# Kernel optimization log

Measured on AMD Instinct MI355X. Metric: run time of the kernel, lower is better.

Reference implementation:

```python
import jax, jax.numpy as jnp
import numpy as np
import math

B, T, D = 8, 1024, 1024
N, L = 256, 768
H = 16
TE = 2048  # time_embed_dim
EPS = 1e-5


def _ln(x, g, b):
    mu = jnp.mean(x, axis=-1, keepdims=True)
    var = jnp.mean(jnp.square(x - mu), axis=-1, keepdims=True)
    return (x - mu) * jax.lax.rsqrt(var + EPS) * g + b


def setup_inputs() -> dict:
    key = jax.random.key(0)
    ks = jax.random.split(key, 16)
    s = lambda fan_in: 1.0 / math.sqrt(fan_in)
    return {
        "x": jax.random.normal(ks[0], (B, T, D), jnp.float32),
        "xf": jax.random.normal(ks[1], (B, N, L), jnp.float32),
        "emb": jax.random.normal(ks[2], (B, TE), jnp.float32),
        "ln_g": jnp.ones((D,), jnp.float32),
        "ln_b": jnp.zeros((D,), jnp.float32),
        "cln_g": jnp.ones((L,), jnp.float32),
        "cln_b": jnp.zeros((L,), jnp.float32),
        "Wq": jax.random.normal(ks[3], (D, D), jnp.float32) * s(D),
        "bq": jnp.zeros((D,), jnp.float32),
        "Wk": jax.random.normal(ks[4], (L, D), jnp.float32) * s(L),
        "bk": jnp.zeros((D,), jnp.float32),
        "Wv": jax.random.normal(ks[5], (L, D), jnp.float32) * s(L),
        "bv": jnp.zeros((D,), jnp.float32),
        "sln_g": jnp.ones((D,), jnp.float32),
        "sln_b": jnp.zeros((D,), jnp.float32),
        "Wemb": jax.random.normal(ks[6], (TE, 2 * D), jnp.float32) * s(TE),
        "bemb": jnp.zeros((2 * D,), jnp.float32),
        "Wout": jax.random.normal(ks[7], (D, D), jnp.float32) * s(D) * 0.02,
        "bout": jnp.zeros((D,), jnp.float32),
    }


def reference(x, xf, emb, ln_g, ln_b, cln_g, cln_b, Wq, bq, Wk, bk, Wv, bv,
              sln_g, sln_b, Wemb, bemb, Wout, bout):
    # x: (B,T,D), xf: (B,N,L), emb: (B,TE)
    hd = D // H
    q = (_ln(x, ln_g, ln_b) @ Wq + bq).reshape(B, T, H, hd)
    xf_n = _ln(xf, cln_g, cln_b)
    k = (xf_n @ Wk + bk).reshape(B, N, H, hd)
    v = (xf_n @ Wv + bv).reshape(B, N, H, hd)
    # scores: (B,T,N,H); note: scaled by sqrt(D//H)
    att = jnp.einsum('bthd,bnhd->btnh', q, k) / math.sqrt(hd)
    w = jax.nn.softmax(att, axis=2)  # softmax over conditioning tokens N
    y = jnp.einsum('btnh,bnhd->bthd', w, v).reshape(B, T, D)
    # StylizationBlock (dropout = 0)
    emb_out = jax.nn.silu(emb) @ Wemb + bemb  # (B, 2D)
    scale, shift = jnp.split(emb_out[:, None, :], 2, axis=2)
    h = _ln(y, sln_g, sln_b) * (1.0 + scale) + shift
    h = jax.nn.silu(h) @ Wout + bout
    return x + h
```

## Files before the change

### kernel.cpp

```cpp
#include <hip/hip_runtime.h>
#include <hip/hip_bf16.h>

typedef __hip_bfloat16 bf16;
typedef unsigned short ushort;
typedef unsigned char uchar;
typedef long i64;
typedef __attribute__((ext_vector_type(4))) float f32x4;

#define B_ 8
#define T_ 1024
#define D_ 1024
#define N_ 256
#define L_ 768
#define H_ 16
#define HD_ 64
#define TE_ 2048

__device__ __forceinline__ void gld16(const void* g, void* l) {
    __builtin_amdgcn_global_load_lds((const __attribute__((address_space(1))) void*)g,
                                     (__attribute__((address_space(3))) void*)l,
                                     16, 0, 0);
}

__device__ __forceinline__ float bitf(unsigned u) { return __uint_as_float(u); }

__device__ __forceinline__ int pk4_fp8(float a, float b, float c, float d) {
    int p = __builtin_amdgcn_cvt_pk_fp8_f32(a, b, 0, false);
    p = __builtin_amdgcn_cvt_pk_fp8_f32(c, d, p, true);
    return p;
}
__device__ __forceinline__ uchar pk1_fp8(float a) {
    int p = __builtin_amdgcn_cvt_pk_fp8_f32(a, a, 0, false);
    return (uchar)(p & 0xff);
}
__device__ __forceinline__ float dec8(uchar b) {
    int e = (b >> 3) & 15, m = b & 7;
    float mag = e ? (float)(8 + m) * bitf((unsigned)(117 + e) << 23)
                  : (float)m * bitf(118u << 23);
    return (b & 0x80) ? -mag : mag;
}

__global__ __launch_bounds__(256) void prep_kernel(
        const float* __restrict__ x, const float* __restrict__ xf,
        const float* __restrict__ g1, const float* __restrict__ b1,
        const float* __restrict__ g2, const float* __restrict__ b2,
        const float* __restrict__ Wq, const float* __restrict__ Wk,
        const float* __restrict__ Wv, const float* __restrict__ Wo,
        const float* __restrict__ emb, const float* __restrict__ Wemb,
        uchar* __restrict__ xn8, uchar* __restrict__ xfn8,
        uchar* __restrict__ wq8, uchar* __restrict__ wk8,
        uchar* __restrict__ wv8, uchar* __restrict__ wo8,
        float* __restrict__ part) {
    __shared__ __align__(16) char smem[16384];
    int bid = blockIdx.x;
    int tid = threadIdx.x;
    if (bid < 10240) {
        const float *rp, *g, *bb; uchar* op; int cols;
        if (bid < B_ * T_) {
            rp = x + (size_t)bid * D_; g = g1; bb = b1; op = xn8 + (size_t)bid * D_; cols = D_;
        } else {
            int r = bid - B_ * T_;
            rp = xf + (size_t)r * L_; g = g2; bb = b2; op = xfn8 + (size_t)r * L_; cols = L_;
        }
        float* ps  = (float*)smem;
        float* ps2 = ps + 4;
        float* st  = ps + 8;
        bool act = tid * 4 < cols;
        float4 v = act ? *(const float4*)&rp[tid * 4] : make_float4(0.f, 0.f, 0.f, 0.f);
        float s = v.x + v.y + v.z + v.w;
        float s2 = v.x * v.x + v.y * v.y + v.z * v.z + v.w * v.w;
        for (int off = 32; off; off >>= 1) {
            s  += __shfl_down(s,  off, 64);
            s2 += __shfl_down(s2, off, 64);
        }
        int wid = tid >> 6, lid = tid & 63;
        if (lid == 0) { ps[wid] = s; ps2[wid] = s2; }
        __syncthreads();
        if (tid == 0) {
            float t = ps[0] + ps[1] + ps[2] + ps[3];
            float t2 = ps2[0] + ps2[1] + ps2[2] + ps2[3];
            float m = t / cols;
            float var = t2 / cols - m * m;
            st[0] = m; st[1] = rsqrtf(var + 1e-5f);
        }
        __syncthreads();
        if (!act) return;
        float mu = st[0], rstd = st[1];
        float4 gv = *(const float4*)&g[tid * 4];
        float4 bv = *(const float4*)&bb[tid * 4];
        float o0 = (v.x - mu) * rstd * gv.x + bv.x;
        float o1 = (v.y - mu) * rstd * gv.y + bv.y;
        float o2 = (v.z - mu) * rstd * gv.z + bv.z;
        float o3 = (v.w - mu) * rstd * gv.w + bv.w;
        *(int*)&op[tid * 4] = pk4_fp8(o0, o1, o2, o3);
    } else if (bid < 11136) {
        uchar (*t)[65] = (uchar(*)[65])smem;
        int id = bid - 10240;
        int xb = id & 15, y = id >> 4;
        const float* W; uchar* Wt; int K, ky;
        if (y < 16)      { W = Wq; Wt = wq8; K = 1024; ky = y; }
        else if (y < 28) { W = Wk; Wt = wk8; K = 768;  ky = y - 16; }
        else if (y < 40) { W = Wv; Wt = wv8; K = 768;  ky = y - 28; }
        else             { W = Wo; Wt = wo8; K = 1024; ky = y - 40; }
        int k0 = ky * 64, n0 = xb * 64;
#pragma unroll
        for (int i = 0; i < 16; i++) {
            int e = tid + i * 256;
            int r = e >> 6, c = e & 63;
            t[r][c] = pk1_fp8(W[(size_t)(k0 + r) * D_ + n0 + c]);
        }
        __syncthreads();
#pragma unroll
        for (int i = 0; i < 4; i++) {
            int e = tid + i * 256;
            int r = e >> 4, cg = (e & 15) * 4;
            unsigned u = (unsigned)t[cg][r] | ((unsigned)t[cg + 1][r] << 8)
                       | ((unsigned)t[cg + 2][r] << 16) | ((unsigned)t[cg + 3][r] << 24);
            *(unsigned*)&Wt[(size_t)(n0 + r) * K + k0 + cg] = u;
        }
    } else {
        float* se  = (float*)smem;
        float* red = (float*)(smem + 8192);
        int id = bid - 11136;
        int j0 = (id & 31) * 64;
        int ks = id >> 5;
        int tx = tid & 15, ty = tid >> 4;
        int w = tid >> 6, lane = tid & 63;
#pragma unroll
        for (int b = 0; b < 8; b++) {
            float xv = emb[b * TE_ + ks * 256 + tid];
            se[b * 256 + tid] = xv / (1.f + __expf(-xv));
        }
        __syncthreads();
        float acc[8][4] = {};
#pragma unroll 4
        for (int i = 0; i < 16; i++) {
            int e = ty + 16 * i;
            float4 wv = *(const float4*)&Wemb[(size_t)(ks * 256 + e) * 2048 + j0 + tx * 4];
#pragma unroll
            for (int b = 0; b < 8; b++) {
                float s = se[b * 256 + e];
                acc[b][0] += s * wv.x; acc[b][1] += s * wv.y;
                acc[b][2] += s * wv.z; acc[b][3] += s * wv.w;
            }
        }
#pragma unroll
        for (int b = 0; b < 8; b++)
#pragma unroll
            for (int m = 0; m < 4; m++) {
                float v = acc[b][m];
                v += __shfl_down(v, 32, 64);
                v += __shfl_down(v, 16, 64);
                if (lane < 16) red[(w * 8 + b) * 64 + lane * 4 + m] = v;
            }
        __syncthreads();
        for (int o = tid; o < 512; o += 256) {
            int b = o >> 6, jl = o & 63;
            float s = red[(0 * 8 + b) * 64 + jl] + red[(1 * 8 + b) * 64 + jl]
                    + red[(2 * 8 + b) * 64 + jl] + red[(3 * 8 + b) * 64 + jl];
            part[((size_t)ks * 8 + b) * 2048 + j0 + jl] = s;
        }
    }
}

template <int MODE>
__device__ __forceinline__ void gemm_body(const uchar* __restrict__ Ap,
                                          const uchar* __restrict__ Bp,
                                          const float* __restrict__ bias,
                                          const float* __restrict__ res,
                                          void* __restrict__ Cout,
                                          int m0, int n0, int Ncols, int K,
                                          uchar* Ash, uchar* Bsh) {
    int tid = threadIdx.x;
    int w = tid >> 6, lane = tid & 63;
    int quad = lane >> 4, l15 = lane & 15;
    int wm = (w >> 1) * 64, wn = (w & 1) * 64;
    int lr8 = lane >> 3;
    int sc  = lane & 7;
    int gc  = sc ^ lr8;
    f32x4 acc[4][4] = {};
    for (int kt = 0; kt < K; kt += 128) {
#pragma unroll
        for (int j = 0; j < 4; j++) {
            int rbase = w * 32 + j * 8;
            gld16(&Ap[(size_t)(m0 + rbase + lr8) * K + kt + gc * 16], &Ash[rbase * 128]);
        }
#pragma unroll
        for (int j = 0; j < 4; j++) {
            int rbase = w * 32 + j * 8;
            gld16(&Bp[(size_t)(n0 + rbase + lr8) * K + kt + gc * 16], &Bsh[rbase * 128]);
        }
        __syncthreads();
#pragma unroll
        for (int kh = 0; kh < 4; kh++) {
            int c4 = kh * 2 + (quad >> 1);
            int sub = (quad & 1) * 8;
            int pos = (c4 ^ (l15 & 7)) * 16 + sub;
            i64 af[4], bfr[4];
#pragma unroll
            for (int mt = 0; mt < 4; mt++)
                af[mt] = *(const i64*)&Ash[(wm + mt * 16 + l15) * 128 + pos];
#pragma unroll
            for (int nt = 0; nt < 4; nt++)
                bfr[nt] = *(const i64*)&Bsh[(wn + nt * 16 + l15) * 128 + pos];
#pragma unroll
            for (int mt = 0; mt < 4; mt++)
#pragma unroll
                for (int nt = 0; nt < 4; nt++)
                    acc[mt][nt] = __builtin_amdgcn_mfma_f32_16x16x32_fp8_fp8(af[mt], bfr[nt], acc[mt][nt], 0, 0, 0);
        }
        __syncthreads();
    }
#pragma unroll
    for (int mt = 0; mt < 4; mt++) {
#pragma unroll
        for (int nt = 0; nt < 4; nt++) {
#pragma unroll
            for (int reg = 0; reg < 4; reg++) {
                int row = m0 + wm + mt * 16 + quad * 4 + reg;
                int col = n0 + wn + nt * 16 + l15;
                float v = acc[mt][nt][reg] + bias[col];
                if (MODE == 1) {
                    v += res[(size_t)row * Ncols + col];
                    ((float*)Cout)[(size_t)row * Ncols + col] = v;
                } else if (MODE == 0) {
                    ((uchar*)Cout)[(size_t)row * Ncols + col] = pk1_fp8(v);
                } else {
                    int b = row >> 8, n = row & 255;
                    int h = col >> 6, d = col & 63;
                    size_t addr = ((size_t)(b * 16 + h)) * 16384 + (size_t)d * 256
                                + (((n >> 4) ^ (d & 15)) * 16) + (n & 15);
                    ((uchar*)Cout)[addr] = pk1_fp8(v);
                }
            }
        }
    }
}

__global__ __launch_bounds__(256) void qkv_gemm(const uchar* __restrict__ xn8,
                                                const uchar* __restrict__ xfn8,
                                                const uchar* __restrict__ wq8,
                                                const uchar* __restrict__ wk8,
                                                const uchar* __restrict__ wv8,
                                                const float* __restrict__ bq,
                                                const float* __restrict__ bk,
                                                const float* __restrict__ bv,
                                                uchar* __restrict__ q8,
                                                uchar* __restrict__ k8,
                                                uchar* __restrict__ vT8,
                                                const float* __restrict__ part,
                                                const float* __restrict__ bemb,
                                                float* __restrict__ embo) {
    __shared__ __align__(16) uchar Ash[128 * 128];
    __shared__ __align__(16) uchar Bsh[128 * 128];
    int bid = blockIdx.x;
    if (bid < 512) {
        gemm_body<0>(xn8, wq8, bq, nullptr, q8,
                     (bid & 63) * 128, (bid >> 6) * 128, D_, D_, Ash, Bsh);
    } else if (bid < 640) {
        int id = bid - 512;
        gemm_body<0>(xfn8, wk8, bk, nullptr, k8,
                     (id & 15) * 128, (id >> 4) * 128, D_, L_, Ash, Bsh);
    } else if (bid < 768) {
        int id = bid - 640;
        gemm_body<2>(xfn8, wv8, bv, nullptr, vT8,
                     (id & 15) * 128, (id >> 4) * 128, D_, L_, Ash, Bsh);
    } else {
        int o = (bid - 768) * 256 + threadIdx.x;
        int b = o >> 11, j = o & 2047;
        float s = bemb[j];
#pragma unroll
        for (int ks = 0; ks < 8; ks++) s += part[((size_t)ks * 8 + b) * 2048 + j];
        embo[o] = s;
    }
}

__global__ __launch_bounds__(256) void out_gemm(const uchar* __restrict__ a8,
                                                const uchar* __restrict__ wo8,
                                                const float* __restrict__ bout,
                                                const float* __restrict__ x,
                                                float* __restrict__ out) {
    __shared__ __align__(16) uchar Ash[128 * 128];
    __shared__ __align__(16) uchar Bsh[128 * 128];
    int bid = blockIdx.x;
    gemm_body<1>(a8, wo8, bout, x, out,
                 (bid & 63) * 128, (bid >> 6) * 128, D_, D_, Ash, Bsh);
}

__global__ __launch_bounds__(256) void attn_mfma(const uchar* __restrict__ q8,
                                                 const uchar* __restrict__ k8,
                                                 const uchar* __restrict__ vT8,
                                                 uchar* __restrict__ y8) {
    __shared__ __align__(16) uchar KV[16384];
    __shared__ __align__(16) uchar P[16384];
    int tid = threadIdx.x;
    int w = tid >> 6, lane = tid & 63;
    int quad = lane >> 4, l15 = lane & 15;
    int t0 = blockIdx.x * 64;
    int bh = blockIdx.y;
    int b = bh >> 4, h = bh & 15;
    int lln = lane >> 3, sp = lane & 7;

#pragma unroll
    for (int j = 0; j < 4; j++) {
        int dn = w * 32 + j * 8 + lln;
        int c8 = sp ^ (dn & 7);
        int n = dn * 2 + (c8 >> 2);
        gld16(&k8[(size_t)(b * N_ + n) * D_ + h * 64 + (c8 & 3) * 16],
              &KV[(w * 32 + j * 8) * 128]);
    }
#pragma unroll
    for (int j = 0; j < 2; j++) {
        int r = w * 16 + j * 8 + lln;
        int c = (sp ^ (r & 7)) & 3;
        gld16(&q8[(size_t)(b * T_ + t0 + r) * D_ + h * 64 + c * 16],
              &P[(w * 16 + j * 8) * 128]);
    }
    __syncthreads();

    int qrow = w * 16 + l15;
    i64 aq[2];
#pragma unroll
    for (int kk2 = 0; kk2 < 2; kk2++) {
        int chunk = kk2 * 2 + (quad >> 1);
        aq[kk2] = *(const i64*)&P[qrow * 128 + ((chunk ^ (qrow & 7)) * 16) + (quad & 1) * 8];
    }
    f32x4 sf[16];
#pragma unroll
    for (int nt = 0; nt < 16; nt++) {
        int n = nt * 16 + l15;
        int dn = n >> 1, hn = n & 1;
        int c80 = (hn * 4 + 0 + (quad >> 1)) ^ (dn & 7);
        int c81 = (hn * 4 + 2 + (quad >> 1)) ^ (dn & 7);
        i64 b0 = *(const i64*)&KV[dn * 128 + c80 * 16 + (quad & 1) * 8];
        i64 b1 = *(const i64*)&KV[dn * 128 + c81 * 16 + (quad & 1) * 8];
        f32x4 z = {};
        f32x4 t = __builtin_amdgcn_mfma_f32_16x16x32_fp8_fp8(aq[0], b0, z, 0, 0, 0);
        sf[nt] = __builtin_amdgcn_mfma_f32_16x16x32_fp8_fp8(aq[1], b1, t, 0, 0, 0);
    }
    __syncthreads();

    const uchar* vbase = vT8 + (size_t)(b * 16 + h) * 16384;
#pragma unroll
    for (int j = 0; j < 4; j++) {
        gld16(&vbase[(w * 4 + j) * 1024 + lane * 16], &KV[(w * 4 + j) * 1024]);
    }

    const float scale = 0.125f;
    float sm[4] = {0.f, 0.f, 0.f, 0.f};
#pragma unroll
    for (int nt = 0; nt < 16; nt++)
#pragma unroll
        for (int reg = 0; reg < 4; reg++) {
            float e = __expf(sf[nt][reg] * scale);
            sf[nt][reg] = e;
            sm[reg] += e;
        }
#pragma unroll
    for (int off = 1; off < 16; off <<= 1)
#pragma unroll
        for (int reg = 0; reg < 4; reg++)
            sm[reg] += __shfl_xor(sm[reg], off, 64);
    float inv[4];
#pragma unroll
    for (int reg = 0; reg < 4; reg++) inv[reg] = 1.f / sm[reg];

#pragma unroll
    for (int nt = 0; nt < 16; nt++)
#pragma unroll
        for (int reg = 0; reg < 4; reg++) {
            int r = w * 16 + quad * 4 + reg;
            int n = nt * 16 + l15;
            P[r * 256 + (((n >> 4) ^ (r & 15)) * 16) + (n & 15)] = pk1_fp8(sf[nt][reg]);
        }
    __syncthreads();

    f32x4 of[4] = {};
    int prow = w * 16 + l15;
#pragma unroll
    for (int kk = 0; kk < 8; kk++) {
        int ck = kk * 2 + (quad >> 1);
        i64 ap = *(const i64*)&P[prow * 256 + ((ck ^ (prow & 15)) * 16) + (quad & 1) * 8];
#pragma unroll
        for (int dt = 0; dt < 4; dt++) {
            int d = dt * 16 + l15;
            i64 bv = *(const i64*)&KV[d * 256 + ((ck ^ (d & 15)) * 16) + (quad & 1) * 8];
            of[dt] = __builtin_amdgcn_mfma_f32_16x16x32_fp8_fp8(ap, bv, of[dt], 0, 0, 0);
        }
    }
#pragma unroll
    for (int dt = 0; dt < 4; dt++)
#pragma unroll
        for (int reg = 0; reg < 4; reg++) {
            int r = t0 + w * 16 + quad * 4 + reg;
            y8[(size_t)(b * T_ + r) * D_ + h * 64 + dt * 16 + l15] =
                pk1_fp8(of[dt][reg] * inv[reg]);
        }
}

__global__ __launch_bounds__(256) void styl_kernel(const uchar* __restrict__ y8,
                                                   const float* __restrict__ g,
                                                   const float* __restrict__ bb,
                                                   const float* __restrict__ embo,
                                                   uchar* __restrict__ a8) {
    int row = blockIdx.x;
    int b = row >> 10;
    int tid = threadIdx.x;
    const uchar* rp = y8 + (size_t)row * D_;
    uchar4 uy = *(const uchar4*)&rp[tid * 4];
    float v0 = dec8(uy.x), v1 = dec8(uy.y), v2 = dec8(uy.z), v3 = dec8(uy.w);
    float s = v0 + v1 + v2 + v3;
    float s2 = v0 * v0 + v1 * v1 + v2 * v2 + v3 * v3;
    for (int off = 32; off; off >>= 1) {
        s  += __shfl_down(s,  off, 64);
        s2 += __shfl_down(s2, off, 64);
    }
    __shared__ float ps[4], ps2[4];
    __shared__ float smu, srstd;
    int wid = tid >> 6, lid = tid & 63;
    if (lid == 0) { ps[wid] = s; ps2[wid] = s2; }
    __syncthreads();
    if (tid == 0) {
        float t = ps[0] + ps[1] + ps[2] + ps[3];
        float t2 = ps2[0] + ps2[1] + ps2[2] + ps2[3];
        float m = t / D_;
        float var = t2 / D_ - m * m;
        smu = m; srstd = rsqrtf(var + 1e-5f);
    }
    __syncthreads();
    float mu = smu, rstd = srstd;
    float4 gv = *(const float4*)&g[tid * 4];
    float4 bv = *(const float4*)&bb[tid * 4];
    float4 scv = *(const float4*)&embo[b * 2048 + tid * 4];
    float4 shv = *(const float4*)&embo[b * 2048 + 1024 + tid * 4];
    float n0 = (v0 - mu) * rstd * gv.x + bv.x;
    float n1 = (v1 - mu) * rstd * gv.y + bv.y;
    float n2 = (v2 - mu) * rstd * gv.z + bv.z;
    float n3 = (v3 - mu) * rstd * gv.w + bv.w;
    float h0 = n0 * (1.f + scv.x) + shv.x;
    float h1 = n1 * (1.f + scv.y) + shv.y;
    float h2 = n2 * (1.f + scv.z) + shv.z;
    float h3 = n3 * (1.f + scv.w) + shv.w;
    h0 = h0 / (1.f + __expf(-h0));
    h1 = h1 / (1.f + __expf(-h1));
    h2 = h2 / (1.f + __expf(-h2));
    h3 = h3 / (1.f + __expf(-h3));
    *(int*)&a8[(size_t)row * D_ + tid * 4] = pk4_fp8(h0, h1, h2, h3);
}

extern "C" void kernel_launch(void* const* d_in, const int* in_sizes, int n_in,
                              void* d_out, int out_size, void* d_ws, size_t ws_size,
                              hipStream_t stream) {
    const float* x    = (const float*)d_in[0];
    const float* xf   = (const float*)d_in[1];
    const float* emb  = (const float*)d_in[2];
    const float* ln_g = (const float*)d_in[3];
    const float* ln_b = (const float*)d_in[4];
    const float* cln_g= (const float*)d_in[5];
    const float* cln_b= (const float*)d_in[6];
    const float* Wq   = (const float*)d_in[7];
    const float* bq   = (const float*)d_in[8];
    const float* Wk   = (const float*)d_in[9];
    const float* bk   = (const float*)d_in[10];
    const float* Wv   = (const float*)d_in[11];
    const float* bv   = (const float*)d_in[12];
    const float* sln_g= (const float*)d_in[13];
    const float* sln_b= (const float*)d_in[14];
    const float* Wemb = (const float*)d_in[15];
    const float* bemb = (const float*)d_in[16];
    const float* Wout = (const float*)d_in[17];
    const float* bout = (const float*)d_in[18];
    float* out = (float*)d_out;

    char* wsp = (char*)d_ws;
    const size_t MB = 1024 * 1024;
    uchar* xn8  = (uchar*)(wsp);
    uchar* xfn8 = (uchar*)(wsp + 8 * MB);
    uchar* wq8  = (uchar*)(wsp + 10 * MB);
    uchar* wk8  = (uchar*)(wsp + 11 * MB);
    uchar* wv8  = (uchar*)(wsp + 12 * MB);
    uchar* wo8  = (uchar*)(wsp + 13 * MB);
    uchar* q8   = (uchar*)(wsp + 14 * MB);
    uchar* k8   = (uchar*)(wsp + 22 * MB);
    uchar* vT8  = (uchar*)(wsp + 24 * MB);
    uchar* y8   = (uchar*)(wsp + 26 * MB);
    uchar* a8   = (uchar*)(wsp + 34 * MB);
    float* embo = (float*)(wsp + 42 * MB);
    float* part = (float*)(wsp + 43 * MB);

    prep_kernel<<<11392, 256, 0, stream>>>(x, xf, ln_g, ln_b, cln_g, cln_b,
                                           Wq, Wk, Wv, Wout, emb, Wemb,
                                           xn8, xfn8, wq8, wk8, wv8, wo8, part);

    qkv_gemm<<<832, 256, 0, stream>>>(xn8, xfn8, wq8, wk8, wv8, bq, bk, bv,
                                      q8, k8, vT8, part, bemb, embo);

    attn_mfma<<<dim3(16, 128), 256, 0, stream>>>(q8, k8, vT8, y8);

    styl_kernel<<<B_ * T_, 256, 0, stream>>>(y8, sln_g, sln_b, embo, a8);

    out_gemm<<<512, 256, 0, stream>>>(a8, wo8, bout, x, out);
}
```

Baseline: 235.7 us.

## Use one wavefront per row for layernorms and stage fp8 outputs through LDS

The prep and stylization layernorm kernels now process one row per 64-lane wavefront with shuffle-only reductions. This removes the shared-memory barriers and quarters the block count. The qkv GEMM's fp8 output (MODE 0) and the attention output are first staged in LDS and then written with 16-byte vector stores instead of scattered byte stores. The attention grid is remapped to 1D with a swizzled block-to-work order, which changes how blocks land on compute units and how they share cache. Each change trades extra LDS traffic and a barrier, or more registers per thread, for better coalescing and less synchronization.

```diff
diff --git a/kernel.cpp b/kernel.cpp
--- a/kernel.cpp
+++ b/kernel.cpp
@@ -38,6 +38,40 @@
     float mag = e ? (float)(8 + m) * bitf((unsigned)(117 + e) << 23)
                   : (float)m * bitf(118u << 23);
     return (b & 0x80) ? -mag : mag;
+}
+
+template <int NV>
+__device__ __forceinline__ void ln_row(const float* __restrict__ rp,
+                                       const float* __restrict__ g,
+                                       const float* __restrict__ bb,
+                                       uchar* __restrict__ op, int lane) {
+    float4 va[NV];
+#pragma unroll
+    for (int i = 0; i < NV; i++) va[i] = ((const float4*)rp)[i * 64 + lane];
+    float s = 0.f, s2 = 0.f;
+#pragma unroll
+    for (int i = 0; i < NV; i++) {
+        s  += va[i].x + va[i].y + va[i].z + va[i].w;
+        s2 += va[i].x * va[i].x + va[i].y * va[i].y + va[i].z * va[i].z + va[i].w * va[i].w;
+    }
+#pragma unroll
+    for (int off = 32; off; off >>= 1) {
+        s  += __shfl_xor(s,  off, 64);
+        s2 += __shfl_xor(s2, off, 64);
+    }
+    const float inv_n = 1.f / (float)(NV * 256);
+    float mu = s * inv_n;
+    float var = s2 * inv_n - mu * mu;
+    float rstd = rsqrtf(var + 1e-5f);
+#pragma unroll
+    for (int i = 0; i < NV; i++) {
+        float4 gv = ((const float4*)g)[i * 64 + lane];
+        float4 bv = ((const float4*)bb)[i * 64 + lane];
+        ((int*)op)[i * 64 + lane] = pk4_fp8((va[i].x - mu) * rstd * gv.x + bv.x,
+                                            (va[i].y - mu) * rstd * gv.y + bv.y,
+                                            (va[i].z - mu) * rstd * gv.z + bv.z,
+                                            (va[i].w - mu) * rstd * gv.w + bv.w);
+    }
 }
 
 __global__ __launch_bounds__(256) void prep_kernel(
@@ -54,48 +88,18 @@
     __shared__ __align__(16) char smem[16384];
     int bid = blockIdx.x;
     int tid = threadIdx.x;
-    if (bid < 10240) {
-        const float *rp, *g, *bb; uchar* op; int cols;
-        if (bid < B_ * T_) {
-            rp = x + (size_t)bid * D_; g = g1; bb = b1; op = xn8 + (size_t)bid * D_; cols = D_;
+    if (bid < 2560) {
+        int w = tid >> 6, lane = tid & 63;
+        int row = bid * 4 + w;
+        if (row < B_ * T_) {
+            ln_row<4>(x + (size_t)row * D_, g1, b1, xn8 + (size_t)row * D_, lane);
         } else {
-            int r = bid - B_ * T_;
-            rp = xf + (size_t)r * L_; g = g2; bb = b2; op = xfn8 + (size_t)r * L_; cols = L_;
-        }
-        float* ps  = (float*)smem;
-        float* ps2 = ps + 4;
-        float* st  = ps + 8;
-        bool act = tid * 4 < cols;
-        float4 v = act ? *(const float4*)&rp[tid * 4] : make_float4(0.f, 0.f, 0.f, 0.f);
-        float s = v.x + v.y + v.z + v.w;
-        float s2 = v.x * v.x + v.y * v.y + v.z * v.z + v.w * v.w;
-        for (int off = 32; off; off >>= 1) {
-            s  += __shfl_down(s,  off, 64);
-            s2 += __shfl_down(s2, off, 64);
-        }
-        int wid = tid >> 6, lid = tid & 63;
-        if (lid == 0) { ps[wid] = s; ps2[wid] = s2; }
-        __syncthreads();
-        if (tid == 0) {
-            float t = ps[0] + ps[1] + ps[2] + ps[3];
-            float t2 = ps2[0] + ps2[1] + ps2[2] + ps2[3];
-            float m = t / cols;
-            float var = t2 / cols - m * m;
-            st[0] = m; st[1] = rsqrtf(var + 1e-5f);
-        }
-        __syncthreads();
-        if (!act) return;
-        float mu = st[0], rstd = st[1];
-        float4 gv = *(const float4*)&g[tid * 4];
-        float4 bv = *(const float4*)&bb[tid * 4];
-        float o0 = (v.x - mu) * rstd * gv.x + bv.x;
-        float o1 = (v.y - mu) * rstd * gv.y + bv.y;
-        float o2 = (v.z - mu) * rstd * gv.z + bv.z;
-        float o3 = (v.w - mu) * rstd * gv.w + bv.w;
-        *(int*)&op[tid * 4] = pk4_fp8(o0, o1, o2, o3);
-    } else if (bid < 11136) {
+            int r = row - B_ * T_;
+            ln_row<3>(xf + (size_t)r * L_, g2, b2, xfn8 + (size_t)r * L_, lane);
+        }
+    } else if (bid < 3456) {
         uchar (*t)[65] = (uchar(*)[65])smem;
-        int id = bid - 10240;
+        int id = bid - 2560;
         int xb = id & 15, y = id >> 4;
         const float* W; uchar* Wt; int K, ky;
         if (y < 16)      { W = Wq; Wt = wq8; K = 1024; ky = y; }
@@ -121,7 +125,7 @@
     } else {
         float* se  = (float*)smem;
         float* red = (float*)(smem + 8192);
-        int id = bid - 11136;
+        int id = bid - 3456;
         int j0 = (id & 31) * 64;
         int ks = id >> 5;
         int tx = tid & 15, ty = tid >> 4;
@@ -211,26 +215,45 @@
         }
         __syncthreads();
     }
-#pragma unroll
-    for (int mt = 0; mt < 4; mt++) {
-#pragma unroll
-        for (int nt = 0; nt < 4; nt++) {
-#pragma unroll
-            for (int reg = 0; reg < 4; reg++) {
-                int row = m0 + wm + mt * 16 + quad * 4 + reg;
-                int col = n0 + wn + nt * 16 + l15;
-                float v = acc[mt][nt][reg] + bias[col];
-                if (MODE == 1) {
-                    v += res[(size_t)row * Ncols + col];
-                    ((float*)Cout)[(size_t)row * Ncols + col] = v;
-                } else if (MODE == 0) {
-                    ((uchar*)Cout)[(size_t)row * Ncols + col] = pk1_fp8(v);
-                } else {
-                    int b = row >> 8, n = row & 255;
-                    int h = col >> 6, d = col & 63;
-                    size_t addr = ((size_t)(b * 16 + h)) * 16384 + (size_t)d * 256
-                                + (((n >> 4) ^ (d & 15)) * 16) + (n & 15);
-                    ((uchar*)Cout)[addr] = pk1_fp8(v);
+    if (MODE == 0) {
+#pragma unroll
+        for (int mt = 0; mt < 4; mt++)
+#pragma unroll
+            for (int nt = 0; nt < 4; nt++)
+#pragma unroll
+                for (int reg = 0; reg < 4; reg++) {
+                    int rl = wm + mt * 16 + quad * 4 + reg;
+                    int cl = wn + nt * 16 + l15;
+                    Ash[rl * 128 + cl] = pk1_fp8(acc[mt][nt][reg] + bias[n0 + cl]);
+                }
+        __syncthreads();
+#pragma unroll
+        for (int i = 0; i < 4; i++) {
+            int row = (tid >> 3) + i * 32;
+            int ch = (tid & 7) * 16;
+            *(int4*)&((uchar*)Cout)[(size_t)(m0 + row) * Ncols + n0 + ch] =
+                *(const int4*)&Ash[row * 128 + ch];
+        }
+    } else {
+#pragma unroll
+        for (int mt = 0; mt < 4; mt++) {
+#pragma unroll
+            for (int nt = 0; nt < 4; nt++) {
+#pragma unroll
+                for (int reg = 0; reg < 4; reg++) {
+                    int row = m0 + wm + mt * 16 + quad * 4 + reg;
+                    int col = n0 + wn + nt * 16 + l15;
+                    float v = acc[mt][nt][reg] + bias[col];
+                    if (MODE == 1) {
+                        v += res[(size_t)row * Ncols + col];
+                        ((float*)Cout)[(size_t)row * Ncols + col] = v;
+                    } else {
+                        int b = row >> 8, n = row & 255;
+                        int h = col >> 6, d = col & 63;
+                        size_t addr = ((size_t)(b * 16 + h)) * 16384 + (size_t)d * 256
+                                    + (((n >> 4) ^ (d & 15)) * 16) + (n & 15);
+                        ((uchar*)Cout)[addr] = pk1_fp8(v);
+                    }
                 }
             }
         }
@@ -296,8 +319,10 @@
     int tid = threadIdx.x;
     int w = tid >> 6, lane = tid & 63;
     int quad = lane >> 4, l15 = lane & 15;
-    int t0 = blockIdx.x * 64;
-    int bh = blockIdx.y;
+    int bid = blockIdx.x;
+    int work = (bid & 7) * 256 + (bid >> 3);
+    int t0 = (work & 15) * 64;
+    int bh = work >> 4;
     int b = bh >> 4, h = bh & 15;
     int lln = lane >> 3, sp = lane & 7;
 
@@ -388,14 +413,20 @@
             of[dt] = __builtin_amdgcn_mfma_f32_16x16x32_fp8_fp8(ap, bv, of[dt], 0, 0, 0);
         }
     }
+    __syncthreads();
 #pragma unroll
     for (int dt = 0; dt < 4; dt++)
 #pragma unroll
         for (int reg = 0; reg < 4; reg++) {
-            int r = t0 + w * 16 + quad * 4 + reg;
-            y8[(size_t)(b * T_ + r) * D_ + h * 64 + dt * 16 + l15] =
-                pk1_fp8(of[dt][reg] * inv[reg]);
-        }
+            int rl = w * 16 + quad * 4 + reg;
+            P[rl * 64 + dt * 16 + l15] = pk1_fp8(of[dt][reg] * inv[reg]);
+        }
+    __syncthreads();
+    {
+        int row = tid >> 2, ch = (tid & 3) * 16;
+        *(int4*)&y8[(size_t)(b * T_ + t0 + row) * D_ + h * 64 + ch] =
+            *(const int4*)&P[row * 64 + ch];
+    }
 }
 
 __global__ __launch_bounds__(256) void styl_kernel(const uchar* __restrict__ y8,
@@ -403,49 +434,50 @@
                                                    const float* __restrict__ bb,
                                                    const float* __restrict__ embo,
                                                    uchar* __restrict__ a8) {
-    int row = blockIdx.x;
+    int tid = threadIdx.x, w = tid >> 6, lane = tid & 63;
+    int row = blockIdx.x * 4 + w;
     int b = row >> 10;
-    int tid = threadIdx.x;
     const uchar* rp = y8 + (size_t)row * D_;
-    uchar4 uy = *(const uchar4*)&rp[tid * 4];
-    float v0 = dec8(uy.x), v1 = dec8(uy.y), v2 = dec8(uy.z), v3 = dec8(uy.w);
-    float s = v0 + v1 + v2 + v3;
-    float s2 = v0 * v0 + v1 * v1 + v2 * v2 + v3 * v3;
+    uchar* op = a8 + (size_t)row * D_;
+    float v[16];
+    float s = 0.f, s2 = 0.f;
+#pragma unroll
+    for (int i = 0; i < 4; i++) {
+        unsigned u = ((const unsigned*)rp)[i * 64 + lane];
+#pragma unroll
+        for (int j = 0; j < 4; j++) {
+            float f = dec8((uchar)(u >> (8 * j)));
+            v[i * 4 + j] = f; s += f; s2 += f * f;
+        }
+    }
+#pragma unroll
     for (int off = 32; off; off >>= 1) {
-        s  += __shfl_down(s,  off, 64);
-        s2 += __shfl_down(s2, off, 64);
-    }
-    __shared__ float ps[4], ps2[4];
-    __shared__ float smu, srstd;
-    int wid = tid >> 6, lid = tid & 63;
-    if (lid == 0) { ps[wid] = s; ps2[wid] = s2; }
-    __syncthreads();
-    if (tid == 0) {
-        float t = ps[0] + ps[1] + ps[2] + ps[3];
-        float t2 = ps2[0] + ps2[1] + ps2[2] + ps2[3];
-        float m = t / D_;
-        float var = t2 / D_ - m * m;
-        smu = m; srstd = rsqrtf(var + 1e-5f);
-    }
-    __syncthreads();
-    float mu = smu, rstd = srstd;
-    float4 gv = *(const float4*)&g[tid * 4];
-    float4 bv = *(const float4*)&bb[tid * 4];
-    float4 scv = *(const float4*)&embo[b * 2048 + tid * 4];
-    float4 shv = *(const float4*)&embo[b * 2048 + 1024 + tid * 4];
-    float n0 = (v0 - mu) * rstd * gv.x + bv.x;
-    float n1 = (v1 - mu) * rstd * gv.y + bv.y;
-    float n2 = (v2 - mu) * rstd * gv.z + bv.z;
-    float n3 = (v3 - mu) * rstd * gv.w + bv.w;
-    float h0 = n0 * (1.f + scv.x) + shv.x;
-    float h1 = n1 * (1.f + scv.y) + shv.y;
-    float h2 = n2 * (1.f + scv.z) + shv.z;
-    float h3 = n3 * (1.f + scv.w) + shv.w;
-    h0 = h0 / (1.f + __expf(-h0));
-    h1 = h1 / (1.f + __expf(-h1));
-    h2 = h2 / (1.f + __expf(-h2));
-    h3 = h3 / (1.f + __expf(-h3));
-    *(int*)&a8[(size_t)row * D_ + tid * 4] = pk4_fp8(h0, h1, h2, h3);
+        s  += __shfl_xor(s,  off, 64);
+        s2 += __shfl_xor(s2, off, 64);
+    }
+    float mu = s * (1.f / 1024.f);
+    float rstd = rsqrtf(s2 * (1.f / 1024.f) - mu * mu + 1e-5f);
+#pragma unroll
+    for (int i = 0; i < 4; i++) {
+        int c4 = i * 64 + lane;
+        float4 gv  = ((const float4*)g)[c4];
+        float4 bv  = ((const float4*)bb)[c4];
+        float4 scv = ((const float4*)(embo + b * 2048))[c4];
+        float4 shv = ((const float4*)(embo + b * 2048 + 1024))[c4];
+        float h0 = (v[i*4+0] - mu) * rstd * gv.x + bv.x;
+        float h1 = (v[i*4+1] - mu) * rstd * gv.y + bv.y;
+        float h2 = (v[i*4+2] - mu) * rstd * gv.z + bv.z;
+        float h3 = (v[i*4+3] - mu) * rstd * gv.w + bv.w;
+        h0 = h0 * (1.f + scv.x) + shv.x;
+        h1 = h1 * (1.f + scv.y) + shv.y;
+        h2 = h2 * (1.f + scv.z) + shv.z;
+        h3 = h3 * (1.f + scv.w) + shv.w;
+        h0 = h0 / (1.f + __expf(-h0));
+        h1 = h1 / (1.f + __expf(-h1));
+        h2 = h2 / (1.f + __expf(-h2));
+        h3 = h3 / (1.f + __expf(-h3));
+        ((int*)op)[c4] = pk4_fp8(h0, h1, h2, h3);
+    }
 }
 
 extern "C" void kernel_launch(void* const* d_in, const int* in_sizes, int n_in,
@@ -488,16 +520,16 @@
     float* embo = (float*)(wsp + 42 * MB);
     float* part = (float*)(wsp + 43 * MB);
 
-    prep_kernel<<<11392, 256, 0, stream>>>(x, xf, ln_g, ln_b, cln_g, cln_b,
-                                           Wq, Wk, Wv, Wout, emb, Wemb,
-                                           xn8, xfn8, wq8, wk8, wv8, wo8, part);
+    prep_kernel<<<3712, 256, 0, stream>>>(x, xf, ln_g, ln_b, cln_g, cln_b,
+                                          Wq, Wk, Wv, Wout, emb, Wemb,
+                                          xn8, xfn8, wq8, wk8, wv8, wo8, part);
 
     qkv_gemm<<<832, 256, 0, stream>>>(xn8, xfn8, wq8, wk8, wv8, bq, bk, bv,
                                       q8, k8, vT8, part, bemb, embo);
 
-    attn_mfma<<<dim3(16, 128), 256, 0, stream>>>(q8, k8, vT8, y8);
-
-    styl_kernel<<<B_ * T_, 256, 0, stream>>>(y8, sln_g, sln_b, embo, a8);
+    attn_mfma<<<2048, 256, 0, stream>>>(q8, k8, vT8, y8);
+
+    styl_kernel<<<2048, 256, 0, stream>>>(y8, sln_g, sln_b, embo, a8);
 
     out_gemm<<<512, 256, 0, stream>>>(a8, wo8, bout, x, out);
 }
```

Measured after the change: 229.7 us. 2.6% less time.
